# Kernel tuning notes

Measured on AMD Instinct MI355X. Metric: run time of the kernel, lower is better.

The kernel has to match this reference:

```python
import jax, jax.numpy as jnp
import numpy as np

NUM_CLASSES = 256
DIM_EMB = 11
B, S = 512, 2048


def _dense_params(key, fan_in, fan_out):
    kw, _ = jax.random.split(key)
    lim = np.sqrt(6.0 / (fan_in + fan_out))  # glorot_uniform (keras default)
    W = jax.random.uniform(kw, (fan_in, fan_out), jnp.float32, -lim, lim)
    b = jnp.zeros((fan_out,), jnp.float32)
    return W, b


def setup_inputs() -> dict:
    key = jax.random.key(0)
    ks = jax.random.split(key, 12)
    tokens = jax.random.randint(ks[0], (B, S), 0, NUM_CLASSES, dtype=jnp.int32)
    emb = jax.random.uniform(ks[1], (NUM_CLASSES, DIM_EMB), jnp.float32, -0.05, 0.05)
    W112, b112 = _dense_params(ks[2], DIM_EMB, 2)
    W113, b113 = _dense_params(ks[3], DIM_EMB, 3)
    W115, b115 = _dense_params(ks[4], DIM_EMB, 5)
    W117, b117 = _dense_params(ks[5], DIM_EMB, 7)
    W21, b21 = _dense_params(ks[6], 2, 1)
    W31, b31 = _dense_params(ks[7], 3, 1)
    W51, b51 = _dense_params(ks[8], 5, 1)
    W71, b71 = _dense_params(ks[9], 7, 1)
    W111, b111 = _dense_params(ks[10], DIM_EMB, 1)
    Wout, bout = _dense_params(ks[11], 73, DIM_EMB)
    return dict(tokens=tokens, emb=emb,
                W112=W112, b112=b112, W113=W113, b113=b113,
                W115=W115, b115=b115, W117=W117, b117=b117,
                W21=W21, b21=b21, W31=W31, b31=b31, W51=W51, b51=b51,
                W71=W71, b71=b71, W111=W111, b111=b111,
                Wout=Wout, bout=bout)


def _forward(tokens, emb, W112, b112, W113, b113, W115, b115, W117, b117,
             W21, b21, W31, b31, W51, b51, W71, b71, W111, b111, Wout, bout):
    sw = jax.nn.swish
    x = emb[tokens]                         # [B,S,11]
    d112 = sw(x @ W112 + b112)              # [B,S,2]
    d113 = sw(x @ W113 + b113)              # [B,S,3]
    d115 = sw(x @ W115 + b115)              # [B,S,5]
    d117 = sw(x @ W117 + b117)              # [B,S,7]
    d21 = sw(d112 @ W21 + b21)              # [B,S,1]
    d31 = sw(d113 @ W31 + b31)
    d51 = sw(d115 @ W51 + b51)
    d71 = sw(d117 @ W71 + b71)
    d111 = sw(x @ W111 + b111)
    singles = [d21, d31, d51, d71, d111]
    pairs = [(0, 1), (0, 2), (0, 3), (0, 4), (1, 2), (1, 3), (1, 4), (2, 3), (2, 4), (3, 4)]
    adds = [singles[i] + singles[j] for i, j in pairs]
    muls = [singles[i] * singles[j] for i, j in pairs]
    mins = [jnp.minimum(singles[i], singles[j]) for i, j in pairs]
    maxs = [jnp.maximum(singles[i], singles[j]) for i, j in pairs]
    cat = jnp.concatenate([x, d112, d113, d115, d117] + singles + adds + muls + mins + maxs, axis=-1)  # [B,S,73]
    return jnp.tanh(cat @ Wout + bout)      # [B,S,11]


def reference(tokens, emb, W112, b112, W113, b113, W115, b115, W117, b117,
              W21, b21, W31, b31, W51, b51, W71, b71, W111, b111, Wout, bout):
    return _forward(tokens, emb, W112, b112, W113, b113, W115, b115, W117, b117,
                    W21, b21, W31, b31, W51, b51, W71, b71, W111, b111, Wout, bout)
```

## Files before the change

kernel.cpp:

```cpp
#include <hip/hip_runtime.h>
#include <hip/hip_bf16.h>

#define NTOK  (512 * 2048)
#define OUTC  11
#define NELEM (NTOK * OUTC)
#define NF4   (NELEM / 4)
#define GBLK  1408
#define GSTEP (GBLK * 256u)

static __device__ __forceinline__ float swishf(float v) { return v / (1.0f + expf(-v)); }

__global__ __launch_bounds__(256) void build_table_k(
    const float* __restrict__ emb,
    const float* __restrict__ W112, const float* __restrict__ b112,
    const float* __restrict__ W113, const float* __restrict__ b113,
    const float* __restrict__ W115, const float* __restrict__ b115,
    const float* __restrict__ W117, const float* __restrict__ b117,
    const float* __restrict__ W21,  const float* __restrict__ b21,
    const float* __restrict__ W31,  const float* __restrict__ b31,
    const float* __restrict__ W51,  const float* __restrict__ b51,
    const float* __restrict__ W71,  const float* __restrict__ b71,
    const float* __restrict__ W111, const float* __restrict__ b111,
    const float* __restrict__ Wout, const float* __restrict__ bout,
    float* __restrict__ table)
{
    const int c = threadIdx.x;

    float x[11];
    #pragma unroll
    for (int k = 0; k < 11; ++k) x[k] = emb[c * 11 + k];

    float d112[2];
    #pragma unroll
    for (int j = 0; j < 2; ++j) {
        float a = b112[j];
        #pragma unroll
        for (int k = 0; k < 11; ++k) a += x[k] * W112[k * 2 + j];
        d112[j] = swishf(a);
    }
    float d113[3];
    #pragma unroll
    for (int j = 0; j < 3; ++j) {
        float a = b113[j];
        #pragma unroll
        for (int k = 0; k < 11; ++k) a += x[k] * W113[k * 3 + j];
        d113[j] = swishf(a);
    }
    float d115[5];
    #pragma unroll
    for (int j = 0; j < 5; ++j) {
        float a = b115[j];
        #pragma unroll
        for (int k = 0; k < 11; ++k) a += x[k] * W115[k * 5 + j];
        d115[j] = swishf(a);
    }
    float d117[7];
    #pragma unroll
    for (int j = 0; j < 7; ++j) {
        float a = b117[j];
        #pragma unroll
        for (int k = 0; k < 11; ++k) a += x[k] * W117[k * 7 + j];
        d117[j] = swishf(a);
    }

    float s[5];
    {
        float a = b21[0] + d112[0] * W21[0] + d112[1] * W21[1];
        s[0] = swishf(a);
    }
    {
        float a = b31[0];
        #pragma unroll
        for (int j = 0; j < 3; ++j) a += d113[j] * W31[j];
        s[1] = swishf(a);
    }
    {
        float a = b51[0];
        #pragma unroll
        for (int j = 0; j < 5; ++j) a += d115[j] * W51[j];
        s[2] = swishf(a);
    }
    {
        float a = b71[0];
        #pragma unroll
        for (int j = 0; j < 7; ++j) a += d117[j] * W71[j];
        s[3] = swishf(a);
    }
    {
        float a = b111[0];
        #pragma unroll
        for (int k = 0; k < 11; ++k) a += x[k] * W111[k];
        s[4] = swishf(a);
    }

    float cat[73];
    int idx = 0;
    #pragma unroll
    for (int k = 0; k < 11; ++k) cat[idx++] = x[k];
    #pragma unroll
    for (int j = 0; j < 2; ++j) cat[idx++] = d112[j];
    #pragma unroll
    for (int j = 0; j < 3; ++j) cat[idx++] = d113[j];
    #pragma unroll
    for (int j = 0; j < 5; ++j) cat[idx++] = d115[j];
    #pragma unroll
    for (int j = 0; j < 7; ++j) cat[idx++] = d117[j];
    #pragma unroll
    for (int i = 0; i < 5; ++i) cat[idx++] = s[i];

    const int PI[10] = {0, 0, 0, 0, 1, 1, 1, 2, 2, 3};
    const int PJ[10] = {1, 2, 3, 4, 2, 3, 4, 3, 4, 4};
    #pragma unroll
    for (int p = 0; p < 10; ++p) cat[idx++] = s[PI[p]] + s[PJ[p]];
    #pragma unroll
    for (int p = 0; p < 10; ++p) cat[idx++] = s[PI[p]] * s[PJ[p]];
    #pragma unroll
    for (int p = 0; p < 10; ++p) cat[idx++] = fminf(s[PI[p]], s[PJ[p]]);
    #pragma unroll
    for (int p = 0; p < 10; ++p) cat[idx++] = fmaxf(s[PI[p]], s[PJ[p]]);

    for (int o = 0; o < 11; ++o) {
        float a = bout[o];
        #pragma unroll
        for (int i = 0; i < 73; ++i) a += cat[i] * Wout[i * 11 + o];
        table[c * 11 + o] = tanhf(a);
    }
}

__global__ __launch_bounds__(256) void gather_k(
    const int* __restrict__ tokens,
    const float* __restrict__ table_g,
    float4* __restrict__ out)
{
    __shared__ float tbl[256 * 11];
    const int tid = threadIdx.x;
    #pragma unroll
    for (int i = tid; i < 256 * 11; i += 256) tbl[i] = table_g[i];
    __syncthreads();

    unsigned int q = blockIdx.x * 256u + (unsigned int)tid;
    #pragma unroll
    for (int k = 0; k < 8; ++k, q += GSTEP) {
        const unsigned int e0 = q * 4u;
        const unsigned int t0 = e0 / 11u;
        const unsigned int r0 = e0 - t0 * 11u;
        unsigned int t1 = t0 + 1u;
        if (t1 >= (unsigned int)NTOK) t1 = NTOK - 1u;

        const unsigned int base0 = (unsigned int)tokens[t0] * 11u;
        const unsigned int base1 = (unsigned int)tokens[t1] * 11u;

        float v[4];
        #pragma unroll
        for (int j = 0; j < 4; ++j) {
            const unsigned int r = r0 + (unsigned int)j;
            const bool second = (r >= 11u);
            const unsigned int idx = second ? (base1 + r - 11u) : (base0 + r);
            v[j] = tbl[idx];
        }

        out[q] = make_float4(v[0], v[1], v[2], v[3]);
    }
}

extern "C" void kernel_launch(void* const* d_in, const int* in_sizes, int n_in,
                              void* d_out, int out_size, void* d_ws, size_t ws_size,
                              hipStream_t stream)
{
    const int* tokens = (const int*)d_in[0];
    #define FP(i) ((const float*)d_in[i])
    float* table = (float*)d_ws;

    build_table_k<<<1, 256, 0, stream>>>(
        FP(1),
        FP(2),  FP(3),  FP(4),  FP(5),
        FP(6),  FP(7),  FP(8),  FP(9),
        FP(10), FP(11), FP(12), FP(13),
        FP(14), FP(15), FP(16), FP(17),
        FP(18), FP(19), FP(20), FP(21),
        table);

    gather_k<<<GBLK, 256, 0, stream>>>(
        tokens, (const float*)d_ws, (float4*)d_out);
    #undef FP
}
```

Before: 134.3 us.

## Fuse table build into gather kernel with per-block recompute and nontemporal stores

Merges the single-block table-building kernel into the gather kernel: each block recomputes the 256x11 output table directly into shared memory, then gathers. This removes a serialized kernel launch and the global table round trip. The grid shrinks to 512 blocks with 22 iterations each, and output writes use nontemporal stores to avoid cache pollution. The trade-off is redundant table computation in every block.

```diff
diff --git a/kernel.cpp b/kernel.cpp
--- a/kernel.cpp
+++ b/kernel.cpp
@@ -5,12 +5,16 @@
 #define OUTC  11
 #define NELEM (NTOK * OUTC)
 #define NF4   (NELEM / 4)
-#define GBLK  1408
+#define GBLK  512
+#define GITER 22
 #define GSTEP (GBLK * 256u)
+
+typedef float v4f __attribute__((ext_vector_type(4)));
 
 static __device__ __forceinline__ float swishf(float v) { return v / (1.0f + expf(-v)); }
 
-__global__ __launch_bounds__(256) void build_table_k(
+__global__ __launch_bounds__(256) void fused_k(
+    const int* __restrict__ tokens,
     const float* __restrict__ emb,
     const float* __restrict__ W112, const float* __restrict__ b112,
     const float* __restrict__ W113, const float* __restrict__ b113,
@@ -22,125 +26,118 @@
     const float* __restrict__ W71,  const float* __restrict__ b71,
     const float* __restrict__ W111, const float* __restrict__ b111,
     const float* __restrict__ Wout, const float* __restrict__ bout,
-    float* __restrict__ table)
-{
-    const int c = threadIdx.x;
-
-    float x[11];
-    #pragma unroll
-    for (int k = 0; k < 11; ++k) x[k] = emb[c * 11 + k];
-
-    float d112[2];
-    #pragma unroll
-    for (int j = 0; j < 2; ++j) {
-        float a = b112[j];
-        #pragma unroll
-        for (int k = 0; k < 11; ++k) a += x[k] * W112[k * 2 + j];
-        d112[j] = swishf(a);
-    }
-    float d113[3];
-    #pragma unroll
-    for (int j = 0; j < 3; ++j) {
-        float a = b113[j];
-        #pragma unroll
-        for (int k = 0; k < 11; ++k) a += x[k] * W113[k * 3 + j];
-        d113[j] = swishf(a);
-    }
-    float d115[5];
-    #pragma unroll
-    for (int j = 0; j < 5; ++j) {
-        float a = b115[j];
-        #pragma unroll
-        for (int k = 0; k < 11; ++k) a += x[k] * W115[k * 5 + j];
-        d115[j] = swishf(a);
-    }
-    float d117[7];
-    #pragma unroll
-    for (int j = 0; j < 7; ++j) {
-        float a = b117[j];
-        #pragma unroll
-        for (int k = 0; k < 11; ++k) a += x[k] * W117[k * 7 + j];
-        d117[j] = swishf(a);
-    }
-
-    float s[5];
-    {
-        float a = b21[0] + d112[0] * W21[0] + d112[1] * W21[1];
-        s[0] = swishf(a);
-    }
-    {
-        float a = b31[0];
-        #pragma unroll
-        for (int j = 0; j < 3; ++j) a += d113[j] * W31[j];
-        s[1] = swishf(a);
-    }
-    {
-        float a = b51[0];
-        #pragma unroll
-        for (int j = 0; j < 5; ++j) a += d115[j] * W51[j];
-        s[2] = swishf(a);
-    }
-    {
-        float a = b71[0];
-        #pragma unroll
-        for (int j = 0; j < 7; ++j) a += d117[j] * W71[j];
-        s[3] = swishf(a);
-    }
-    {
-        float a = b111[0];
-        #pragma unroll
-        for (int k = 0; k < 11; ++k) a += x[k] * W111[k];
-        s[4] = swishf(a);
-    }
-
-    float cat[73];
-    int idx = 0;
-    #pragma unroll
-    for (int k = 0; k < 11; ++k) cat[idx++] = x[k];
-    #pragma unroll
-    for (int j = 0; j < 2; ++j) cat[idx++] = d112[j];
-    #pragma unroll
-    for (int j = 0; j < 3; ++j) cat[idx++] = d113[j];
-    #pragma unroll
-    for (int j = 0; j < 5; ++j) cat[idx++] = d115[j];
-    #pragma unroll
-    for (int j = 0; j < 7; ++j) cat[idx++] = d117[j];
-    #pragma unroll
-    for (int i = 0; i < 5; ++i) cat[idx++] = s[i];
-
-    const int PI[10] = {0, 0, 0, 0, 1, 1, 1, 2, 2, 3};
-    const int PJ[10] = {1, 2, 3, 4, 2, 3, 4, 3, 4, 4};
-    #pragma unroll
-    for (int p = 0; p < 10; ++p) cat[idx++] = s[PI[p]] + s[PJ[p]];
-    #pragma unroll
-    for (int p = 0; p < 10; ++p) cat[idx++] = s[PI[p]] * s[PJ[p]];
-    #pragma unroll
-    for (int p = 0; p < 10; ++p) cat[idx++] = fminf(s[PI[p]], s[PJ[p]]);
-    #pragma unroll
-    for (int p = 0; p < 10; ++p) cat[idx++] = fmaxf(s[PI[p]], s[PJ[p]]);
-
-    for (int o = 0; o < 11; ++o) {
-        float a = bout[o];
-        #pragma unroll
-        for (int i = 0; i < 73; ++i) a += cat[i] * Wout[i * 11 + o];
-        table[c * 11 + o] = tanhf(a);
-    }
-}
-
-__global__ __launch_bounds__(256) void gather_k(
-    const int* __restrict__ tokens,
-    const float* __restrict__ table_g,
-    float4* __restrict__ out)
+    v4f* __restrict__ out)
 {
     __shared__ float tbl[256 * 11];
     const int tid = threadIdx.x;
-    #pragma unroll
-    for (int i = tid; i < 256 * 11; i += 256) tbl[i] = table_g[i];
+
+    {
+        const int c = tid;
+
+        float x[11];
+        #pragma unroll
+        for (int k = 0; k < 11; ++k) x[k] = emb[c * 11 + k];
+
+        float d112[2];
+        #pragma unroll
+        for (int j = 0; j < 2; ++j) {
+            float a = b112[j];
+            #pragma unroll
+            for (int k = 0; k < 11; ++k) a += x[k] * W112[k * 2 + j];
+            d112[j] = swishf(a);
+        }
+        float d113[3];
+        #pragma unroll
+        for (int j = 0; j < 3; ++j) {
+            float a = b113[j];
+            #pragma unroll
+            for (int k = 0; k < 11; ++k) a += x[k] * W113[k * 3 + j];
+            d113[j] = swishf(a);
+        }
+        float d115[5];
+        #pragma unroll
+        for (int j = 0; j < 5; ++j) {
+            float a = b115[j];
+            #pragma unroll
+            for (int k = 0; k < 11; ++k) a += x[k] * W115[k * 5 + j];
+            d115[j] = swishf(a);
+        }
+        float d117[7];
+        #pragma unroll
+        for (int j = 0; j < 7; ++j) {
+            float a = b117[j];
+            #pragma unroll
+            for (int k = 0; k < 11; ++k) a += x[k] * W117[k * 7 + j];
+            d117[j] = swishf(a);
+        }
+
+        float s[5];
+        {
+            float a = b21[0] + d112[0] * W21[0] + d112[1] * W21[1];
+            s[0] = swishf(a);
+        }
+        {
+            float a = b31[0];
+            #pragma unroll
+            for (int j = 0; j < 3; ++j) a += d113[j] * W31[j];
+            s[1] = swishf(a);
+        }
+        {
+            float a = b51[0];
+            #pragma unroll
+            for (int j = 0; j < 5; ++j) a += d115[j] * W51[j];
+            s[2] = swishf(a);
+        }
+        {
+            float a = b71[0];
+            #pragma unroll
+            for (int j = 0; j < 7; ++j) a += d117[j] * W71[j];
+            s[3] = swishf(a);
+        }
+        {
+            float a = b111[0];
+            #pragma unroll
+            for (int k = 0; k < 11; ++k) a += x[k] * W111[k];
+            s[4] = swishf(a);
+        }
+
+        float cat[73];
+        int idx = 0;
+        #pragma unroll
+        for (int k = 0; k < 11; ++k) cat[idx++] = x[k];
+        #pragma unroll
+        for (int j = 0; j < 2; ++j) cat[idx++] = d112[j];
+        #pragma unroll
+        for (int j = 0; j < 3; ++j) cat[idx++] = d113[j];
+        #pragma unroll
+        for (int j = 0; j < 5; ++j) cat[idx++] = d115[j];
+        #pragma unroll
+        for (int j = 0; j < 7; ++j) cat[idx++] = d117[j];
+        #pragma unroll
+        for (int i = 0; i < 5; ++i) cat[idx++] = s[i];
+
+        const int PI[10] = {0, 0, 0, 0, 1, 1, 1, 2, 2, 3};
+        const int PJ[10] = {1, 2, 3, 4, 2, 3, 4, 3, 4, 4};
+        #pragma unroll
+        for (int p = 0; p < 10; ++p) cat[idx++] = s[PI[p]] + s[PJ[p]];
+        #pragma unroll
+        for (int p = 0; p < 10; ++p) cat[idx++] = s[PI[p]] * s[PJ[p]];
+        #pragma unroll
+        for (int p = 0; p < 10; ++p) cat[idx++] = fminf(s[PI[p]], s[PJ[p]]);
+        #pragma unroll
+        for (int p = 0; p < 10; ++p) cat[idx++] = fmaxf(s[PI[p]], s[PJ[p]]);
+
+        for (int o = 0; o < 11; ++o) {
+            float a = bout[o];
+            #pragma unroll
+            for (int i = 0; i < 73; ++i) a += cat[i] * Wout[i * 11 + o];
+            tbl[c * 11 + o] = tanhf(a);
+        }
+    }
     __syncthreads();
 
     unsigned int q = blockIdx.x * 256u + (unsigned int)tid;
-    #pragma unroll
-    for (int k = 0; k < 8; ++k, q += GSTEP) {
+    for (int k = 0; k < GITER; ++k, q += GSTEP) {
         const unsigned int e0 = q * 4u;
         const unsigned int t0 = e0 / 11u;
         const unsigned int r0 = e0 - t0 * 11u;
@@ -159,7 +156,9 @@
             v[j] = tbl[idx];
         }
 
-        out[q] = make_float4(v[0], v[1], v[2], v[3]);
+        v4f o;
+        o.x = v[0]; o.y = v[1]; o.z = v[2]; o.w = v[3];
+        __builtin_nontemporal_store(o, &out[q]);
     }
 }
 
@@ -169,18 +168,15 @@
 {
     const int* tokens = (const int*)d_in[0];
     #define FP(i) ((const float*)d_in[i])
-    float* table = (float*)d_ws;
 
-    build_table_k<<<1, 256, 0, stream>>>(
+    fused_k<<<GBLK, 256, 0, stream>>>(
+        tokens,
         FP(1),
         FP(2),  FP(3),  FP(4),  FP(5),
         FP(6),  FP(7),  FP(8),  FP(9),
         FP(10), FP(11), FP(12), FP(13),
         FP(14), FP(15), FP(16), FP(17),
         FP(18), FP(19), FP(20), FP(21),
-        table);
-
-    gather_k<<<GBLK, 256, 0, stream>>>(
-        tokens, (const float*)d_ws, (float4*)d_out);
+        (v4f*)d_out);
     #undef FP
 }
```

New measurement: 132.6 us. About the same (-1.3%).
